# Kernel tuning notes

Measured on AMD Instinct MI355X. Metric: run time of the kernel, lower is better.

## Reference

```python
import jax, jax.numpy as jnp
import numpy as np

NUM_GROUPS = 32
EPS = 1e-5

def group_norm(x, gamma, beta):
    # x: [B, C, L]
    B, C, L = x.shape
    g = x.reshape(B, NUM_GROUPS, C // NUM_GROUPS, L)
    mu = g.mean(axis=(2, 3), keepdims=True)
    var = g.var(axis=(2, 3), keepdims=True)
    g = (g - mu) * jax.lax.rsqrt(var + EPS)
    h = g.reshape(B, C, L)
    return h * gamma[None, :, None] + beta[None, :, None]

def conv1x1(h, W, b):
    # h: [B, C, L], W: [Cout, Cin], b: [Cout] -> [B, Cout, L]
    return jnp.einsum('oc,bcl->bol', W, h) + b[None, :, None]

def setup_inputs() -> dict:
    key = jax.random.key(0)
    ks = jax.random.split(key, 10)
    B, C, L = 8, 512, 2048
    s = 1.0 / np.sqrt(C)
    inp = {
        'x': jax.random.normal(ks[0], (B, C, L), dtype=jnp.float32),
        'gn_gamma': jnp.ones((C,), jnp.float32),
        'gn_beta': jnp.zeros((C,), jnp.float32),
        'Wq': jax.random.normal(ks[1], (C, C), jnp.float32) * s,
        'bq': jnp.zeros((C,), jnp.float32),
        'Wk': jax.random.normal(ks[2], (C, C), jnp.float32) * s,
        'bk': jnp.zeros((C,), jnp.float32),
        'Wv': jax.random.normal(ks[3], (C, C), jnp.float32) * s,
        'bv': jnp.zeros((C,), jnp.float32),
        'Wo': jax.random.normal(ks[4], (C, C), jnp.float32) * s,
        'bo': jnp.zeros((C,), jnp.float32),
    }
    return inp

def reference(x, gn_gamma, gn_beta, Wq, bq, Wk, bk, Wv, bv, Wo, bo):
    B, C, L = x.shape
    h = group_norm(x, gn_gamma, gn_beta)
    q = conv1x1(h, Wq, bq)  # [B, C, L]
    k = conv1x1(h, Wk, bk)  # [B, C, L]
    v = conv1x1(h, Wv, bv)  # [B, C, L]
    scale = 1.0 / jnp.sqrt(jnp.float32(C)).astype(x.dtype)
    w = jnp.einsum('bci,bcj->bij', q, k) * scale  # [B, L, L]
    w = jax.nn.softmax(w, axis=-1)
    a = jnp.einsum('bij,bcj->bci', w, v)  # [B, C, L]
    return x + conv1x1(a, Wo, bo)
```

## Files before the change

kernel.cpp:

```cpp
#include <hip/hip_runtime.h>
#include <hip/hip_bf16.h>

#define B_ 8
#define C_ 512
#define L_ 2048
#define G_ 32

typedef __attribute__((ext_vector_type(8))) short bf16x8;
typedef __attribute__((ext_vector_type(4))) float f32x4;

__device__ __forceinline__ float b2f(short h) {
    union { unsigned u; float f; } c; c.u = ((unsigned)(unsigned short)h) << 16; return c.f;
}
__device__ __forceinline__ short f2b(float f) {
    union { float f; unsigned u; } c; c.f = f;
    unsigned r = (c.u + 0x7FFFu + ((c.u >> 16) & 1u)) >> 16;
    return (short)r;
}

__device__ __forceinline__ void load_lds16(const void* g, void* s) {
    __builtin_amdgcn_global_load_lds(
        (const __attribute__((address_space(1))) void*)g,
        (__attribute__((address_space(3))) void*)s, 16, 0, 0);
}

template<int N>
__device__ __forceinline__ void wait_vm() {
    if constexpr (N == 0)      asm volatile("s_waitcnt vmcnt(0)" ::: "memory");
    else if constexpr (N == 2) asm volatile("s_waitcnt vmcnt(2)" ::: "memory");
    else if constexpr (N == 6) asm volatile("s_waitcnt vmcnt(6)" ::: "memory");
    else                       asm volatile("s_waitcnt vmcnt(8)" ::: "memory");
    __builtin_amdgcn_sched_barrier(0);
}
__device__ __forceinline__ void wait_lgkm0() {
    asm volatile("s_waitcnt lgkmcnt(0)" ::: "memory");
    __builtin_amdgcn_sched_barrier(0);
}
__device__ __forceinline__ void sbar() {
    __builtin_amdgcn_sched_barrier(0);
    __builtin_amdgcn_s_barrier();
    __builtin_amdgcn_sched_barrier(0);
}

__global__ __launch_bounds__(256) void cvt_w(
    const float* __restrict__ a, const float* __restrict__ b,
    const float* __restrict__ c, const float* __restrict__ d,
    short* __restrict__ o)
{
    const float* src = (blockIdx.y == 0) ? a : (blockIdx.y == 1) ? b
                     : (blockIdx.y == 2) ? c : d;
    short* dst = o + (size_t)blockIdx.y * (C_ * C_);
    int i = (blockIdx.x * 256 + threadIdx.x) * 4;
    float4 v = *(const float4*)(src + i);
    short4 r;
    r.x = f2b(v.x); r.y = f2b(v.y); r.z = f2b(v.z); r.w = f2b(v.w);
    *(short4*)(dst + i) = r;
}

__global__ __launch_bounds__(256) void groupnorm_tr(
    const float* __restrict__ x, const float* __restrict__ gamma,
    const float* __restrict__ beta, short* __restrict__ h_t,
    float* __restrict__ rsum)
{
    __shared__ float xb[16][2052];
    __shared__ float rs[4], rss[4], stats[2], gam[16], bet[16];
    int bg = blockIdx.x;
    int b = bg >> 5, g = bg & 31;
    const float* xg = x + ((size_t)b * C_ + (size_t)g * 16) * L_;
    int t = threadIdx.x;
    if (t < 64) rsum[(size_t)bg * 64 + t] = 0.f;
    float s = 0.f, ss = 0.f;
    #pragma unroll 4
    for (int i = t; i < 8192; i += 256) {
        float4 v = ((const float4*)xg)[i];
        int cl = i >> 9, l4 = (i & 511) << 2;
        *(float4*)&xb[cl][l4] = v;
        s  += v.x + v.y + v.z + v.w;
        ss += v.x * v.x + v.y * v.y + v.z * v.z + v.w * v.w;
    }
    #pragma unroll
    for (int o = 32; o > 0; o >>= 1) { s += __shfl_down(s, o); ss += __shfl_down(ss, o); }
    int wave = t >> 6, lane = t & 63;
    if (lane == 0) { rs[wave] = s; rss[wave] = ss; }
    if (t < 16) { gam[t] = gamma[g * 16 + t]; bet[t] = beta[g * 16 + t]; }
    __syncthreads();
    if (t == 0) {
        float S = rs[0] + rs[1] + rs[2] + rs[3];
        float SS = rss[0] + rss[1] + rss[2] + rss[3];
        float mean = S * (1.f / 32768.f);
        float var = SS * (1.f / 32768.f) - mean * mean;
        stats[0] = mean; stats[1] = rsqrtf(var + 1e-5f);
    }
    __syncthreads();
    float mean = stats[0], rstd = stats[1];
    short* ho = h_t + (size_t)b * L_ * C_ + (size_t)g * 16;
    for (int i = t; i < 32768; i += 256) {
        int cl = i & 15, l = i >> 4;
        float xv = xb[cl][l];
        float hv = (xv - mean) * rstd * gam[cl] + bet[cl];
        ho[(size_t)l * C_ + cl] = f2b(hv);
    }
}

#define MM(mh, nh, bfx)                                                        \
  do {                                                                         \
    _Pragma("unroll") for (int i_ = 0; i_ < 4; i_++)                           \
    _Pragma("unroll") for (int j_ = 0; j_ < 2; j_++)                           \
    _Pragma("unroll") for (int kk_ = 0; kk_ < 2; kk_++)                        \
      acc[(mh)*4 + i_][(nh)*2 + j_] = __builtin_amdgcn_mfma_f32_16x16x32_bf16( \
          af[i_][kk_], bfx[j_][kk_], acc[(mh)*4 + i_][(nh)*2 + j_], 0, 0, 0);  \
  } while (0)

template<int BIAS_MODE, bool EXPSUM>
__global__ __launch_bounds__(512, 2) void gemm8(
    const short* __restrict__ A, const short* __restrict__ Bt,
    void* __restrict__ Co, const float* __restrict__ bias,
    const float* __restrict__ bias2, float* __restrict__ rowsum,
    int K, int lda, int ldb, int ldc,
    long sA, long sB, long sC, float alpha)
{
    __shared__ __align__(16) short As0[256 * 64];
    __shared__ __align__(16) short As1[256 * 64];
    __shared__ __align__(16) short Bs0[256 * 64];
    __shared__ __align__(16) short Bs1[256 * 64];

    int nbx = gridDim.x, nby = gridDim.y, nbz = gridDim.z;
    int lin = blockIdx.x + nbx * (blockIdx.y + nby * blockIdx.z);
    int total = nbx * nby * nbz;
    int bx, by, bz;
    if ((total & 7) == 0) {
        int chunk = total >> 3;
        int logical = (lin & 7) * chunk + (lin >> 3);
        bx = logical % nbx; int t2 = logical / nbx; by = t2 % nby; bz = t2 / nby;
    } else { bx = blockIdx.x; by = blockIdx.y; bz = blockIdx.z; }

    int m0 = by * 256, n0 = bx * 256;
    int t = threadIdx.x, lane = t & 63;
    int wave = t >> 6;
    int wm = wave >> 2, wn = wave & 3;
    int fr = lane & 15, fq = lane >> 4;
    int ch0 = (fq ^ (fr & 7)) << 3;
    int ch1 = ((4 | fq) ^ (fr & 7)) << 3;
    int rs_ = t >> 3, cs_ = t & 7;
    int gcol = ((cs_ ^ (rs_ & 7)) << 3);

    const short* gA = A + (size_t)bz * sA + (size_t)(m0 + rs_) * lda + gcol;
    const short* gB = Bt + (size_t)bz * sB + (size_t)(n0 + rs_) * ldb + gcol;

    f32x4 acc[8][4] = {};
    bf16x8 af[4][2], bf0[2][2], bf1[2][2];

    auto stgA = [&](short* dst, int tile, int h) {
        const short* s = gA + (size_t)(h * 128) * lda + tile * 64;
        load_lds16(s, dst + h * 8192 + t * 8);
        load_lds16(s + (size_t)64 * lda, dst + h * 8192 + 4096 + t * 8);
    };
    auto stgB = [&](short* dst, int tile, int h) {
        const short* s = gB + (size_t)(h * 128) * ldb + tile * 64;
        load_lds16(s, dst + h * 8192 + t * 8);
        load_lds16(s + (size_t)64 * ldb, dst + h * 8192 + 4096 + t * 8);
    };
    auto rdA = [&](const short* S, int mh) {
        #pragma unroll
        for (int i = 0; i < 4; i++) {
            int R = wm * 128 + (mh * 4 + i) * 16 + fr;
            af[i][0] = *(const bf16x8*)(S + R * 64 + ch0);
            af[i][1] = *(const bf16x8*)(S + R * 64 + ch1);
        }
    };
    auto rdB = [&](const short* S, int nh, bf16x8 (&bf)[2][2]) {
        #pragma unroll
        for (int j = 0; j < 2; j++) {
            int R = wn * 64 + (nh * 2 + j) * 16 + fr;
            bf[j][0] = *(const bf16x8*)(S + R * 64 + ch0);
            bf[j][1] = *(const bf16x8*)(S + R * 64 + ch1);
        }
    };

    int nk = K >> 6;

    auto TILE = [&](short* cA, short* cB, short* nA, short* nB, int tt) {
        rdA(cA, 0); rdB(cB, 0, bf0);
        if (tt + 1 < nk) stgA(nA, tt + 1, 1);
        sbar(); wait_lgkm0();
        __builtin_amdgcn_s_setprio(1); MM(0, 0, bf0); __builtin_amdgcn_s_setprio(0);
        sbar();
        rdB(cB, 1, bf1);
        if (tt + 1 < nk) stgB(nB, tt + 1, 0);
        sbar(); wait_lgkm0();
        __builtin_amdgcn_s_setprio(1); MM(0, 1, bf1); __builtin_amdgcn_s_setprio(0);
        sbar();
        rdA(cA, 1);
        if (tt + 1 < nk) stgB(nB, tt + 1, 1);
        sbar(); wait_lgkm0();
        __builtin_amdgcn_s_setprio(1); MM(1, 0, bf0); __builtin_amdgcn_s_setprio(0);
        sbar();
        if (tt + 2 < nk) stgA(cA, tt + 2, 0);
        __builtin_amdgcn_s_setprio(1); MM(1, 1, bf1); __builtin_amdgcn_s_setprio(0);
        if (tt + 2 < nk) wait_vm<2>(); else wait_vm<0>();
        sbar();
    };

    stgA(As0, 0, 0); stgA(As0, 0, 1); stgB(Bs0, 0, 0); stgB(Bs0, 0, 1);
    if (nk > 1) stgA(As1, 1, 0);
    wait_vm<2>();
    sbar();

    for (int tt = 0; tt < nk; tt += 2) {
        TILE(As0, Bs0, As1, Bs1, tt);
        TILE(As1, Bs1, As0, Bs0, tt + 1);
    }

    size_t cb = (size_t)bz * sC;
    int crow = fq * 4;
    float psum[8][4];
    if (EXPSUM) {
        #pragma unroll
        for (int mi = 0; mi < 8; mi++)
            #pragma unroll
            for (int r = 0; r < 4; r++) psum[mi][r] = 0.f;
    }
    #pragma unroll
    for (int mi = 0; mi < 8; mi++) {
        #pragma unroll
        for (int nj = 0; nj < 4; nj++) {
            int n = n0 + wn * 64 + nj * 16 + fr;
            float bn = 0.f;
            if (BIAS_MODE == 3) bn = (n < 512) ? bias[n] : bias2[n - 512];
            #pragma unroll
            for (int r = 0; r < 4; r++) {
                int m = m0 + wm * 128 + mi * 16 + crow + r;
                float v = acc[mi][nj][r] * alpha;
                if (EXPSUM) { v = __expf(v); psum[mi][r] += v; }
                if (BIAS_MODE == 3) v += bn;
                ((short*)Co)[cb + (size_t)m * ldc + n] = f2b(v);
            }
        }
    }
    if (EXPSUM) {
        #pragma unroll
        for (int mi = 0; mi < 8; mi++)
            #pragma unroll
            for (int r = 0; r < 4; r++) {
                float s = psum[mi][r];
                s += __shfl_xor(s, 1); s += __shfl_xor(s, 2);
                s += __shfl_xor(s, 4); s += __shfl_xor(s, 8);
                if ((lane & 15) == 0) {
                    int m = m0 + wm * 128 + mi * 16 + crow + r;
                    atomicAdd(rowsum + (size_t)bz * L_ + m, s);
                }
            }
    }
}

template<int BM, int PIPE, int BIAS_MODE, bool RESID, bool OUTF32, bool EXPSUM, bool ROWDIV>
__global__ __launch_bounds__(BM * 2) void gemm_bt(
    const short* __restrict__ A, const short* __restrict__ Bt,
    void* __restrict__ Co, const float* __restrict__ bias,
    const float* __restrict__ bias2, const float* __restrict__ resid,
    float* __restrict__ rowsum,
    int N, int K, int lda, int ldb, int ldc,
    long sA, long sB, long sC, float alpha)
{
    constexpr int T = BM * 2;
    constexpr int RPP = T / 8;
    constexpr int LPS = BM / RPP + 128 / RPP;
    constexpr int NBUF = (PIPE == 1) ? 2 : 1;
    __shared__ __align__(16) short As[NBUF][BM * 64];
    __shared__ __align__(16) short Bs[NBUF][128 * 64];

    int nbx = gridDim.x, nby = gridDim.y, nbz = gridDim.z;
    int lin = blockIdx.x + nbx * (blockIdx.y + nby * blockIdx.z);
    int total = nbx * nby * nbz;
    int bx, by, bz;
    if ((total & 7) == 0) {
        int chunk = total >> 3;
        int logical = (lin & 7) * chunk + (lin >> 3);
        bx = logical % nbx; int t2 = logical / nbx; by = t2 % nby; bz = t2 / nby;
    } else { bx = blockIdx.x; by = blockIdx.y; bz = blockIdx.z; }

    const short* Ab = A + (size_t)bz * sA;
    const short* Bb = Bt + (size_t)bz * sB;
    int m0 = by * BM, n0 = bx * 128;
    int t = threadIdx.x, lane = t & 63;
    int wave = t >> 6;
    int wm = wave >> 1, wn = wave & 1;

    f32x4 acc[4][4] = {};

    int rs_ = t >> 3, cs_ = t & 7;
    int gcol = ((cs_ ^ (rs_ & 7)) << 3);
    const short* gA = Ab + (size_t)(m0 + rs_) * lda + gcol;
    const short* gB = Bb + (size_t)(n0 + rs_) * ldb + gcol;
    int fr = lane & 15, fq = lane >> 4;
    int ch0 = (fq ^ (fr & 7)) << 3;
    int ch1 = ((4 | fq) ^ (fr & 7)) << 3;

    auto stage = [&](short* Asb, short* Bsb) {
        #pragma unroll
        for (int i = 0; i < BM / RPP; i++)
            load_lds16(gA + (size_t)(RPP * i) * lda, Asb + i * (RPP * 64) + t * 8);
        #pragma unroll
        for (int i = 0; i < 128 / RPP; i++)
            load_lds16(gB + (size_t)(RPP * i) * ldb, Bsb + i * (RPP * 64) + t * 8);
        gA += 64; gB += 64;
    };
    auto compute = [&](const short* Asb, const short* Bsb) {
        #pragma unroll
        for (int kk = 0; kk < 2; kk++) {
            int ch = kk ? ch1 : ch0;
            bf16x8 af[4], bfr[4];
            #pragma unroll
            for (int i = 0; i < 4; i++) {
                int R = wm * 64 + i * 16 + fr;
                af[i] = *(const bf16x8*)(Asb + R * 64 + ch);
            }
            #pragma unroll
            for (int j = 0; j < 4; j++) {
                int R = wn * 64 + j * 16 + fr;
                bfr[j] = *(const bf16x8*)(Bsb + R * 64 + ch);
            }
            #pragma unroll
            for (int mt = 0; mt < 4; mt++)
                #pragma unroll
                for (int nt = 0; nt < 4; nt++)
                    acc[mt][nt] = __builtin_amdgcn_mfma_f32_16x16x32_bf16(
                        af[mt], bfr[nt], acc[mt][nt], 0, 0, 0);
        }
    };

    if constexpr (PIPE == 0) {
        for (int k0 = 0; k0 < K; k0 += 64) {
            __syncthreads();
            stage(As[0], Bs[0]);
            __syncthreads();
            compute(As[0], Bs[0]);
        }
    } else {
        int nk = K >> 6;
        stage(As[0], Bs[0]);
        stage(As[1], Bs[1]);
        wait_vm<LPS>();
        sbar();
        for (int kt = 0; kt < nk; kt += 2) {
            compute(As[0], Bs[0]);
            sbar();
            if (kt + 2 < nk) { stage(As[0], Bs[0]); wait_vm<LPS>(); }
            else               wait_vm<0>();
            sbar();
            compute(As[1], Bs[1]);
            sbar();
            if (kt + 3 < nk) { stage(As[1], Bs[1]); wait_vm<LPS>(); }
            else               wait_vm<0>();
            sbar();
        }
    }

    size_t cb = (size_t)bz * sC;
    int crow = (lane >> 4) * 4;
    int wrow = wm * 64;
    float psum[4][4];
    float inv[4][4];
    if (EXPSUM) {
        #pragma unroll
        for (int mt = 0; mt < 4; mt++)
            #pragma unroll
            for (int r = 0; r < 4; r++) psum[mt][r] = 0.f;
    }
    if (ROWDIV) {
        #pragma unroll
        for (int mt = 0; mt < 4; mt++)
            #pragma unroll
            for (int r = 0; r < 4; r++) {
                int m = m0 + wrow + mt * 16 + crow + r;
                inv[mt][r] = 1.f / rowsum[(size_t)bz * L_ + m];
            }
    }
    #pragma unroll
    for (int mt = 0; mt < 4; mt++) {
        #pragma unroll
        for (int nt = 0; nt < 4; nt++) {
            int n = n0 + wn * 64 + nt * 16 + fr;
            float bn = 0.f;
            if (BIAS_MODE == 3) bn = (n < 512) ? bias[n] : bias2[n - 512];
            #pragma unroll
            for (int r = 0; r < 4; r++) {
                int m = m0 + wrow + mt * 16 + crow + r;
                float v = acc[mt][nt][r] * alpha;
                if (EXPSUM) { v = __expf(v); psum[mt][r] += v; }
                if (ROWDIV) v *= inv[mt][r];
                if (BIAS_MODE == 3) v += bn;
                if (BIAS_MODE == 2) v += bias[m];
                size_t idx = cb + (size_t)m * ldc + n;
                if (RESID) v += resid[idx];
                if (OUTF32) ((float*)Co)[idx] = v;
                else        ((short*)Co)[idx] = f2b(v);
            }
        }
    }
    if (EXPSUM) {
        #pragma unroll
        for (int mt = 0; mt < 4; mt++)
            #pragma unroll
            for (int r = 0; r < 4; r++) {
                float s = psum[mt][r];
                s += __shfl_xor(s, 1); s += __shfl_xor(s, 2);
                s += __shfl_xor(s, 4); s += __shfl_xor(s, 8);
                if ((lane & 15) == 0) {
                    int m = m0 + wrow + mt * 16 + crow + r;
                    atomicAdd(rowsum + (size_t)bz * L_ + m, s);
                }
            }
    }
}

extern "C" void kernel_launch(void* const* d_in, const int* in_sizes, int n_in,
                              void* d_out, int out_size, void* d_ws, size_t ws_size,
                              hipStream_t stream)
{
    const float* x     = (const float*)d_in[0];
    const float* gamma = (const float*)d_in[1];
    const float* beta  = (const float*)d_in[2];
    const float* Wq    = (const float*)d_in[3];
    const float* bq    = (const float*)d_in[4];
    const float* Wk    = (const float*)d_in[5];
    const float* bk    = (const float*)d_in[6];
    const float* Wv    = (const float*)d_in[7];
    const float* bv    = (const float*)d_in[8];
    const float* Wo    = (const float*)d_in[9];
    const float* bo    = (const float*)d_in[10];
    float* out = (float*)d_out;

    const size_t MiB = 1024 * 1024;
    const size_t CC = (size_t)C_ * C_;
    const size_t LC = (size_t)L_ * C_;
    const size_t LL = (size_t)L_ * L_;
    const size_t wbytes = 4 * CC * sizeof(short);

    const size_t perb = 16 * MiB + L_ * sizeof(float);
    int nb = 1;
    for (int c = 8; c >= 1; c >>= 1)
        if (ws_size >= wbytes + (size_t)c * perb) { nb = c; break; }

    short* wq_b = (short*)d_ws;
    short* wv_b = wq_b + 2 * CC;
    short* wo_b = wv_b + CC;
    short* h_t  = wo_b + CC;
    short* qk_t = h_t + (size_t)nb * LC;
    short* v_   = qk_t + (size_t)nb * 2 * LC;
    short* S    = v_  + (size_t)nb * LC;
    float* rsum = (float*)(S + (size_t)nb * LL);
    short* a_t  = h_t;

    const long sLC = (long)LC;
    const long sLL = (long)LL;
    const float scale = 0.044194173824159216f;

    cvt_w<<<dim3(C_ * C_ / 1024, 4), 256, 0, stream>>>(Wq, Wk, Wv, Wo, wq_b);

    for (int b0 = 0; b0 < B_; b0 += nb) {
        const float* xb = x + (size_t)b0 * LC;
        float* outb = out + (size_t)b0 * LC;

        groupnorm_tr<<<dim3(nb * G_), 256, 0, stream>>>(xb, gamma, beta, h_t, rsum);

        gemm8<3, false><<<dim3(4, 8, nb), 512, 0, stream>>>(
            h_t, wq_b, qk_t, bq, bk, nullptr,
            512, 512, 512, 1024, sLC, 0, 2 * sLC, 1.f);
        gemm_bt<128, 1, 2, false, false, false, false><<<dim3(16, 4, nb), 256, 0, stream>>>(
            wv_b, h_t, v_, bv, nullptr, nullptr, nullptr,
            2048, 512, 512, 512, 2048, 0, sLC, sLC, 1.f);
        gemm_bt<256, 0, 0, false, false, true, false><<<dim3(16, 8, nb), 512, 0, stream>>>(
            qk_t, qk_t + 512, S, nullptr, nullptr, nullptr, rsum,
            2048, 512, 1024, 1024, 2048, 2 * sLC, 2 * sLC, sLL, scale);
        gemm_bt<128, 1, 0, false, false, false, true><<<dim3(4, 16, nb), 256, 0, stream>>>(
            S, v_, a_t, nullptr, nullptr, nullptr, rsum,
            512, 2048, 2048, 2048, 512, sLL, sLC, sLC, 1.f);
        gemm_bt<128, 1, 2, true, true, false, false><<<dim3(16, 4, nb), 256, 0, stream>>>(
            wo_b, a_t, outb, bo, nullptr, xb, nullptr,
            2048, 512, 512, 512, 2048, 0, sLC, sLC, 1.f);
    }
}
```

Measured before the change: 273.2 us.

## Retile PV GEMM to 256-row blocks, pack groupnorm stores, fold log2e into exp2

The S·V GEMM moves from 128-row double-buffered tiles with 256 threads to 256-row single-buffered tiles with 512 threads, halving its grid. This raises per-block reuse but gives up the load/compute pipelining. GroupNorm now writes two bf16 channels per 32-bit store, cutting store instructions. The softmax exponent uses exp2f with log2(e) folded into the scale. Dead EXPSUM code is removed from gemm8.

```diff
diff --git a/kernel.cpp b/kernel.cpp
--- a/kernel.cpp
+++ b/kernel.cpp
@@ -9,9 +9,6 @@
 typedef __attribute__((ext_vector_type(8))) short bf16x8;
 typedef __attribute__((ext_vector_type(4))) float f32x4;
 
-__device__ __forceinline__ float b2f(short h) {
-    union { unsigned u; float f; } c; c.u = ((unsigned)(unsigned short)h) << 16; return c.f;
-}
 __device__ __forceinline__ short f2b(float f) {
     union { float f; unsigned u; } c; c.f = f;
     unsigned r = (c.u + 0x7FFFu + ((c.u >> 16) & 1u)) >> 16;
@@ -94,11 +91,13 @@
     __syncthreads();
     float mean = stats[0], rstd = stats[1];
     short* ho = h_t + (size_t)b * L_ * C_ + (size_t)g * 16;
-    for (int i = t; i < 32768; i += 256) {
-        int cl = i & 15, l = i >> 4;
-        float xv = xb[cl][l];
-        float hv = (xv - mean) * rstd * gam[cl] + bet[cl];
-        ho[(size_t)l * C_ + cl] = f2b(hv);
+    for (int i = t; i < 16384; i += 256) {
+        int cp = (i & 7) * 2, l = i >> 3;
+        float a0 = (xb[cp][l]     - mean) * rstd * gam[cp]     + bet[cp];
+        float a1 = (xb[cp + 1][l] - mean) * rstd * gam[cp + 1] + bet[cp + 1];
+        unsigned pk = (unsigned)(unsigned short)f2b(a0)
+                    | ((unsigned)(unsigned short)f2b(a1) << 16);
+        *(unsigned*)(ho + (size_t)l * C_ + cp) = pk;
     }
 }
 
@@ -111,7 +110,7 @@
           af[i_][kk_], bfx[j_][kk_], acc[(mh)*4 + i_][(nh)*2 + j_], 0, 0, 0);  \
   } while (0)
 
-template<int BIAS_MODE, bool EXPSUM>
+template<int BIAS_MODE>
 __global__ __launch_bounds__(512, 2) void gemm8(
     const short* __restrict__ A, const short* __restrict__ Bt,
     void* __restrict__ Co, const float* __restrict__ bias,
@@ -213,13 +212,6 @@
 
     size_t cb = (size_t)bz * sC;
     int crow = fq * 4;
-    float psum[8][4];
-    if (EXPSUM) {
-        #pragma unroll
-        for (int mi = 0; mi < 8; mi++)
-            #pragma unroll
-            for (int r = 0; r < 4; r++) psum[mi][r] = 0.f;
-    }
     #pragma unroll
     for (int mi = 0; mi < 8; mi++) {
         #pragma unroll
@@ -231,25 +223,10 @@
             for (int r = 0; r < 4; r++) {
                 int m = m0 + wm * 128 + mi * 16 + crow + r;
                 float v = acc[mi][nj][r] * alpha;
-                if (EXPSUM) { v = __expf(v); psum[mi][r] += v; }
                 if (BIAS_MODE == 3) v += bn;
                 ((short*)Co)[cb + (size_t)m * ldc + n] = f2b(v);
             }
         }
-    }
-    if (EXPSUM) {
-        #pragma unroll
-        for (int mi = 0; mi < 8; mi++)
-            #pragma unroll
-            for (int r = 0; r < 4; r++) {
-                float s = psum[mi][r];
-                s += __shfl_xor(s, 1); s += __shfl_xor(s, 2);
-                s += __shfl_xor(s, 4); s += __shfl_xor(s, 8);
-                if ((lane & 15) == 0) {
-                    int m = m0 + wm * 128 + mi * 16 + crow + r;
-                    atomicAdd(rowsum + (size_t)bz * L_ + m, s);
-                }
-            }
     }
 }
 
@@ -311,15 +288,11 @@
             int ch = kk ? ch1 : ch0;
             bf16x8 af[4], bfr[4];
             #pragma unroll
-            for (int i = 0; i < 4; i++) {
-                int R = wm * 64 + i * 16 + fr;
-                af[i] = *(const bf16x8*)(Asb + R * 64 + ch);
-            }
-            #pragma unroll
-            for (int j = 0; j < 4; j++) {
-                int R = wn * 64 + j * 16 + fr;
-                bfr[j] = *(const bf16x8*)(Bsb + R * 64 + ch);
-            }
+            for (int i = 0; i < 4; i++)
+                af[i] = *(const bf16x8*)(Asb + (wm * 64 + i * 16 + fr) * 64 + ch);
+            #pragma unroll
+            for (int j = 0; j < 4; j++)
+                bfr[j] = *(const bf16x8*)(Bsb + (wn * 64 + j * 16 + fr) * 64 + ch);
             #pragma unroll
             for (int mt = 0; mt < 4; mt++)
                 #pragma unroll
@@ -387,7 +360,7 @@
             for (int r = 0; r < 4; r++) {
                 int m = m0 + wrow + mt * 16 + crow + r;
                 float v = acc[mt][nt][r] * alpha;
-                if (EXPSUM) { v = __expf(v); psum[mt][r] += v; }
+                if (EXPSUM) { v = exp2f(v); psum[mt][r] += v; }
                 if (ROWDIV) v *= inv[mt][r];
                 if (BIAS_MODE == 3) v += bn;
                 if (BIAS_MODE == 2) v += bias[m];
@@ -454,7 +427,7 @@
 
     const long sLC = (long)LC;
     const long sLL = (long)LL;
-    const float scale = 0.044194173824159216f;
+    const float alpha2 = 0.04419417382415922f * 1.4426950408889634f;
 
     cvt_w<<<dim3(C_ * C_ / 1024, 4), 256, 0, stream>>>(Wq, Wk, Wv, Wo, wq_b);
 
@@ -464,7 +437,7 @@
 
         groupnorm_tr<<<dim3(nb * G_), 256, 0, stream>>>(xb, gamma, beta, h_t, rsum);
 
-        gemm8<3, false><<<dim3(4, 8, nb), 512, 0, stream>>>(
+        gemm8<3><<<dim3(4, 8, nb), 512, 0, stream>>>(
             h_t, wq_b, qk_t, bq, bk, nullptr,
             512, 512, 512, 1024, sLC, 0, 2 * sLC, 1.f);
         gemm_bt<128, 1, 2, false, false, false, false><<<dim3(16, 4, nb), 256, 0, stream>>>(
@@ -472,8 +445,8 @@
             2048, 512, 512, 512, 2048, 0, sLC, sLC, 1.f);
         gemm_bt<256, 0, 0, false, false, true, false><<<dim3(16, 8, nb), 512, 0, stream>>>(
             qk_t, qk_t + 512, S, nullptr, nullptr, nullptr, rsum,
-            2048, 512, 1024, 1024, 2048, 2 * sLC, 2 * sLC, sLL, scale);
-        gemm_bt<128, 1, 0, false, false, false, true><<<dim3(4, 16, nb), 256, 0, stream>>>(
+            2048, 512, 1024, 1024, 2048, 2 * sLC, 2 * sLC, sLL, alpha2);
+        gemm_bt<256, 0, 0, false, false, false, true><<<dim3(4, 8, nb), 512, 0, stream>>>(
             S, v_, a_t, nullptr, nullptr, nullptr, rsum,
             512, 2048, 2048, 2048, 512, sLL, sLC, sLC, 1.f);
         gemm_bt<128, 1, 2, true, true, false, false><<<dim3(16, 4, nb), 256, 0, stream>>>(
```

After: 285.9 us. 4.7% more time.
